# Optimization experiments

Hardware: AMD Instinct MI355X
Metric: run time of the kernel (lower is better)

The kernel has to match this reference:

```python
import jax, jax.numpy as jnp
import numpy as np

VOCAB = 100000
EMB = 256
HID = 512
H = HID // 2            # per-direction hidden size
T_LEN = 2048
N_TAGS = 7
START, END = 5, 6
NEG = -10000.0


def setup_inputs() -> dict:
    key = jax.random.key(0)
    ks = jax.random.split(key, 16)
    n = lambda k, sh: jax.random.normal(k, sh, dtype=jnp.float32)
    bound = 1.0 / np.sqrt(H)  # torch LSTM/Linear-style init scale
    u = lambda k, sh: jax.random.uniform(k, sh, dtype=jnp.float32, minval=-bound, maxval=bound)
    transitions = n(ks[12], (N_TAGS, N_TAGS))
    transitions = transitions.at[:, START].set(NEG).at[END, :].set(NEG)
    return {
        "words": jax.random.randint(ks[0], (T_LEN,), 0, VOCAB),
        "embed": n(ks[1], (VOCAB + 1, EMB)),
        "W_ih_f": u(ks[2], (4 * H, EMB)),
        "W_hh_f": u(ks[3], (4 * H, H)),
        "b_ih_f": u(ks[4], (4 * H,)),
        "b_hh_f": u(ks[5], (4 * H,)),
        "W_ih_b": u(ks[6], (4 * H, EMB)),
        "W_hh_b": u(ks[7], (4 * H, H)),
        "b_ih_b": u(ks[8], (4 * H,)),
        "b_hh_b": u(ks[9], (4 * H,)),
        "W_out": u(ks[10], (N_TAGS, HID)),
        "b_out": u(ks[11], (N_TAGS,)),
        "transitions": transitions,
        "h0": n(ks[13], (2, H)),
        "c0": n(ks[14], (2, H)),
    }


def _lstm_dir(xs, h0, c0, Wih, Whh, bih, bhh):
    # xs: [T, EMB]; torch gate order i, f, g, o
    def step(carry, x):
        h, c = carry
        g = x @ Wih.T + bih + h @ Whh.T + bhh  # [4H]
        i, f, gg, o = jnp.split(g, 4)
        i, f, o = jax.nn.sigmoid(i), jax.nn.sigmoid(f), jax.nn.sigmoid(o)
        c = f * c + i * jnp.tanh(gg)
        h = o * jnp.tanh(c)
        return (h, c), h
    _, hs = jax.lax.scan(step, (h0, c0), xs)
    return hs  # [T, H]


def _features(words, embed, W_ih_f, W_hh_f, b_ih_f, b_hh_f,
              W_ih_b, W_hh_b, b_ih_b, b_hh_b, W_out, b_out, h0, c0):
    xs = embed[words]                                   # [T, EMB]
    hs_f = _lstm_dir(xs, h0[0], c0[0], W_ih_f, W_hh_f, b_ih_f, b_hh_f)
    hs_b = _lstm_dir(xs[::-1], h0[1], c0[1], W_ih_b, W_hh_b, b_ih_b, b_hh_b)[::-1]
    lstm_out = jnp.concatenate([hs_f, hs_b], axis=1)    # [T, HID]
    return lstm_out @ W_out.T + b_out                   # [T, N_TAGS]


def _viterbi(feats, transitions):
    init = jnp.full((N_TAGS,), NEG, dtype=feats.dtype).at[START].set(0.0)

    def vit_step(fv, feat):
        # torch code: next_tag_var[j] = forward_var + transitions[j]
        M = fv[None, :] + transitions          # [j, i] = fv[i] + T[j, i]
        bp = jnp.argmax(M, axis=1)             # [N_TAGS] best prev tag
        fv_new = jnp.max(M, axis=1) + feat
        return fv_new, bp

    fv, bptrs = jax.lax.scan(vit_step, init, feats)     # bptrs: [T, N_TAGS]
    terminal = fv + transitions[END]
    final_tag = jnp.argmax(terminal)
    path_score = terminal[final_tag]

    def back_step(tag, bp):
        return bp[tag], tag
    _start, path = jax.lax.scan(back_step, final_tag, bptrs, reverse=True)
    return path_score, path  # path: [T] tag ids (B/I/E/S/N = 0..4)


def reference(words, embed, W_ih_f, W_hh_f, b_ih_f, b_hh_f,
              W_ih_b, W_hh_b, b_ih_b, b_hh_b, W_out, b_out,
              transitions, h0, c0):
    feats = _features(words, embed, W_ih_f, W_hh_f, b_ih_f, b_hh_f,
                      W_ih_b, W_hh_b, b_ih_b, b_hh_b, W_out, b_out, h0, c0)
    return _viterbi(feats, transitions)
```

## Files before the change

### kernel.cpp

```cpp
#include <hip/hip_runtime.h>

typedef unsigned int u32;

#define T_LEN 2048
#define NEG (-10000.0f)
#define WSCALE 2032.0f
#define HSCALE 127.0f
#define SCALE_INV (1.0f / (2032.0f * 127.0f))

__device__ __forceinline__ int sdot4(u32 a, u32 b, int c) {
#if __has_builtin(__builtin_amdgcn_sdot4)
  return __builtin_amdgcn_sdot4((int)a, (int)b, c, false);
#else
  int r = c;
  r += (int)(signed char)(a)       * (int)(signed char)(b);
  r += (int)(signed char)(a >> 8)  * (int)(signed char)(b >> 8);
  r += (int)(signed char)(a >> 16) * (int)(signed char)(b >> 16);
  r += (int)(signed char)(a >> 24) * (int)(signed char)(b >> 24);
  return r;
#endif
}

__device__ __forceinline__ u32 rdlane_u32(u32 v, int lane) {
#if __has_builtin(__builtin_amdgcn_readlane)
  return (u32)__builtin_amdgcn_readlane((int)v, lane);
#else
  return (u32)__shfl((int)v, lane);
#endif
}

__device__ __forceinline__ float rdlane_f32(float v, int lane) {
  return __builtin_bit_cast(float, rdlane_u32(__builtin_bit_cast(u32, v), lane));
}

__device__ __forceinline__ void block_sync_lds() {
  asm volatile("s_waitcnt lgkmcnt(0)" ::: "memory");
  __builtin_amdgcn_s_barrier();
}

__global__ void pack_whh_i8(const float* __restrict__ Wf,
                            const float* __restrict__ Wb,
                            u32* __restrict__ WP) {
  int idx = blockIdx.x * 256 + threadIdx.x;
  int d   = idx >> 16;
  int G   = (idx >> 14) & 3;
  int q4  = (idx >> 10) & 15;
  int c   = (idx >> 2) & 255;
  int j   = idx & 3;
  const float* W = d ? Wb : Wf;
  float4 v = *(const float4*)&W[(G * 256 + c) * 256 + q4 * 16 + j * 4];
  int b0 = (int)rintf(fminf(fmaxf(v.x * WSCALE, -127.f), 127.f));
  int b1 = (int)rintf(fminf(fmaxf(v.y * WSCALE, -127.f), 127.f));
  int b2 = (int)rintf(fminf(fmaxf(v.z * WSCALE, -127.f), 127.f));
  int b3 = (int)rintf(fminf(fmaxf(v.w * WSCALE, -127.f), 127.f));
  WP[(((d * 4 + G) * 16 + q4) * 256 + c) * 4 + j] =
      (u32)(b0 & 255) | ((u32)(b1 & 255) << 8) |
      ((u32)(b2 & 255) << 16) | ((u32)(b3 & 255) << 24);
}

__global__ void gather_kernel(const int* __restrict__ words,
                              const float* __restrict__ embed,
                              float* __restrict__ xs) {
  int t = blockIdx.x;
  int k = threadIdx.x;
  xs[t * 256 + k] = embed[(size_t)words[t] * 256 + k];
}

__global__ __launch_bounds__(256) void gemm_xw(
    const float* __restrict__ xs,
    const float* __restrict__ Wf, const float* __restrict__ Wb,
    const float* __restrict__ bihf, const float* __restrict__ bhhf,
    const float* __restrict__ bihb, const float* __restrict__ bhhb,
    float* __restrict__ XW) {
  __shared__ float lx[32 * 256];
  __shared__ float lw[32 * 132];
  const int tid = threadIdx.x;
  const int t0 = blockIdx.x * 32;
  const int g0 = blockIdx.y * 128;
  const int d  = blockIdx.z;
  const float* W = d ? Wb : Wf;

  #pragma unroll 4
  for (int r = 0; r < 32; ++r) lx[r * 256 + tid] = xs[(t0 + r) * 256 + tid];

  const int tg = tid & 31, tt = tid >> 5;
  float acc[4][4] = {};

  for (int kc = 0; kc < 8; ++kc) {
    __syncthreads();
    #pragma unroll
    for (int r2 = 0; r2 < 16; ++r2) {
      int gg = r2 * 8 + (tid >> 5);
      int k  = tid & 31;
      lw[k * 132 + gg] = W[(g0 + gg) * 256 + kc * 32 + k];
    }
    __syncthreads();
    #pragma unroll
    for (int k = 0; k < 32; ++k) {
      float4 wv = *(const float4*)&lw[k * 132 + tg * 4];
      #pragma unroll
      for (int a = 0; a < 4; ++a) {
        float xa = lx[(tt * 4 + a) * 256 + kc * 32 + k];
        acc[a][0] = fmaf(xa, wv.x, acc[a][0]);
        acc[a][1] = fmaf(xa, wv.y, acc[a][1]);
        acc[a][2] = fmaf(xa, wv.z, acc[a][2]);
        acc[a][3] = fmaf(xa, wv.w, acc[a][3]);
      }
    }
  }
  const float* bih = d ? bihb : bihf;
  const float* bhh = d ? bhhb : bhhf;
  int gcol = g0 + tg * 4;
  float4 bb;
  bb.x = bih[gcol + 0] + bhh[gcol + 0];
  bb.y = bih[gcol + 1] + bhh[gcol + 1];
  bb.z = bih[gcol + 2] + bhh[gcol + 2];
  bb.w = bih[gcol + 3] + bhh[gcol + 3];
  #pragma unroll
  for (int a = 0; a < 4; ++a) {
    float4 o;
    o.x = acc[a][0] + bb.x;
    o.y = acc[a][1] + bb.y;
    o.z = acc[a][2] + bb.z;
    o.w = acc[a][3] + bb.w;
    *(float4*)&XW[((size_t)d * T_LEN + t0 + tt * 4 + a) * 1024 + gcol] = o;
  }
}

__global__ void __launch_bounds__(256)
__attribute__((amdgpu_waves_per_eu(1, 1)))
lstm_seq(
    const float* __restrict__ XW, float* __restrict__ HS,
    const u32* __restrict__ wpack,
    const float* __restrict__ h0, const float* __restrict__ c0) {
  __shared__ u32 H8[2][64];
  const int tid = threadIdx.x;
  const int d = blockIdx.x;
  const int lane = tid & 63;

  u32 wIv[64], wFv[64], wGv[64], wOv[64];
  {
    const uint4* wr = (const uint4*)wpack;
    #pragma unroll
    for (int q4 = 0; q4 < 16; ++q4) {
      uint4 t;
      t = wr[((d * 4 + 0) * 16 + q4) * 256 + tid];
      wIv[q4 * 4 + 0] = t.x; wIv[q4 * 4 + 1] = t.y;
      wIv[q4 * 4 + 2] = t.z; wIv[q4 * 4 + 3] = t.w;
      t = wr[((d * 4 + 1) * 16 + q4) * 256 + tid];
      wFv[q4 * 4 + 0] = t.x; wFv[q4 * 4 + 1] = t.y;
      wFv[q4 * 4 + 2] = t.z; wFv[q4 * 4 + 3] = t.w;
      t = wr[((d * 4 + 2) * 16 + q4) * 256 + tid];
      wGv[q4 * 4 + 0] = t.x; wGv[q4 * 4 + 1] = t.y;
      wGv[q4 * 4 + 2] = t.z; wGv[q4 * 4 + 3] = t.w;
      t = wr[((d * 4 + 3) * 16 + q4) * 256 + tid];
      wOv[q4 * 4 + 0] = t.x; wOv[q4 * 4 + 1] = t.y;
      wOv[q4 * 4 + 2] = t.z; wOv[q4 * 4 + 3] = t.w;
    }
  }

  float c = c0[d * 256 + tid];
  float h = h0[d * 256 + tid];
  {
    int hi = (int)rintf(fminf(fmaxf(h, -1.0f), 1.0f) * HSCALE);
    ((unsigned char*)&H8[0][0])[tid] = (unsigned char)(hi & 255);
  }
  block_sync_lds();
  u32 hA = H8[0][lane];

  const int delta = d ? -1024 : 1024;
  const float* xwp = XW + ((size_t)d * T_LEN + (d ? (T_LEN - 1) : 0)) * 1024 + tid;
  float xi = xwp[0], xf = xwp[256], xg = xwp[512], xo = xwp[768];

  for (int s = 0; s < T_LEN; ++s) {
    float ni = 0.f, nf = 0.f, ng = 0.f, no = 0.f;
    if (s < T_LEN - 1) {
      xwp += delta;
      ni = xwp[0]; nf = xwp[256]; ng = xwp[512]; no = xwp[768];
    }

    int aI = 0, aF = 0, aG = 0, aO = 0;
    #pragma unroll
    for (int q = 0; q < 64; ++q) {
      u32 sv = rdlane_u32(hA, q);
      aI = sdot4(wIv[q], sv, aI);
      aF = sdot4(wFv[q], sv, aF);
      aG = sdot4(wGv[q], sv, aG);
      aO = sdot4(wOv[q], sv, aO);
    }

    float gi = fmaf((float)aI, SCALE_INV, xi);
    float gf = fmaf((float)aF, SCALE_INV, xf);
    float gc = fmaf((float)aG, SCALE_INV, xg);
    float go = fmaf((float)aO, SCALE_INV, xo);
    gi = 1.0f / (1.0f + __expf(-gi));
    gf = 1.0f / (1.0f + __expf(-gf));
    go = 1.0f / (1.0f + __expf(-go));
    gc = 1.0f - 2.0f / (__expf(2.0f * gc) + 1.0f);
    c = gf * c + gi * gc;
    float th = 1.0f - 2.0f / (__expf(2.0f * c) + 1.0f);
    h = go * th;

    const int t = d ? (T_LEN - 1 - s) : s;
    HS[((size_t)d * T_LEN + t) * 256 + tid] = h;

    int hi = (int)rintf(h * HSCALE);
    const int wbuf = (s + 1) & 1;
    ((unsigned char*)&H8[wbuf][0])[tid] = (unsigned char)(hi & 255);
    block_sync_lds();
    hA = H8[wbuf][lane];
    xi = ni; xf = nf; xg = ng; xo = no;
  }
}

__global__ void feats_kernel(const float* __restrict__ hs,
                             const float* __restrict__ wout,
                             const float* __restrict__ bout,
                             float* __restrict__ feats) {
  __shared__ float lf[16 * 257];
  __shared__ float lb[16 * 257];
  const int tid = threadIdx.x;
  const int t0 = blockIdx.x * 16;
  for (int i = tid; i < 16 * 256; i += 128) {
    int r = i >> 8, k = i & 255;
    lf[r * 257 + k] = hs[(size_t)(t0 + r) * 256 + k];
    lb[r * 257 + k] = hs[(size_t)T_LEN * 256 + (size_t)(t0 + r) * 256 + k];
  }
  __syncthreads();
  const int tl = tid >> 3, n = tid & 7;
  if (n < 7) {
    float acc = bout[n];
    #pragma unroll 8
    for (int k = 0; k < 256; ++k) acc = fmaf(lf[tl * 257 + k], wout[n * 512 + k], acc);
    #pragma unroll 8
    for (int k = 0; k < 256; ++k) acc = fmaf(lb[tl * 257 + k], wout[n * 512 + 256 + k], acc);
    feats[(t0 + tl) * 7 + n] = acc;
  }
}

__global__ __launch_bounds__(256) void viterbi_kernel(
    const float* __restrict__ feats,
    const float* __restrict__ trans,
    float* __restrict__ out) {
  extern __shared__ char vsm[];
  float*         fe = (float*)vsm;
  unsigned char* bp = (unsigned char*)(vsm + 57344);
  unsigned char* G  = (unsigned char*)(vsm + 73728);
  unsigned char* bt = (unsigned char*)(vsm + 73984);
  const int tid = threadIdx.x;

  for (int i = tid; i < T_LEN * 7; i += 256) fe[i] = feats[i];
  __syncthreads();

  if (tid < 64) {
    const int j  = tid;
    const int jc = (j < 7) ? j : 0;
    float Trow[7];
    #pragma unroll
    for (int i = 0; i < 7; ++i) Trow[i] = trans[jc * 7 + i];
    float fv = (j == 5) ? 0.0f : NEG;
    for (int t = 0; t < T_LEN; ++t) {
      float f0 = rdlane_f32(fv, 0), f1 = rdlane_f32(fv, 1), f2 = rdlane_f32(fv, 2),
            f3 = rdlane_f32(fv, 3), f4 = rdlane_f32(fv, 4), f5 = rdlane_f32(fv, 5),
            f6 = rdlane_f32(fv, 6);
      float v0 = f0 + Trow[0], v1 = f1 + Trow[1], v2 = f2 + Trow[2],
            v3 = f3 + Trow[3], v4 = f4 + Trow[4], v5 = f5 + Trow[5],
            v6 = f6 + Trow[6];
      bool c01 = v0 >= v1;  float m01 = c01 ? v0 : v1;  int i01 = c01 ? 0 : 1;
      bool c23 = v2 >= v3;  float m23 = c23 ? v2 : v3;  int i23 = c23 ? 2 : 3;
      bool c45 = v4 >= v5;  float m45 = c45 ? v4 : v5;  int i45 = c45 ? 4 : 5;
      bool cA  = m01 >= m23; float mA = cA ? m01 : m23; int iA = cA ? i01 : i23;
      bool cB  = m45 >= v6;  float mB = cB ? m45 : v6;  int iB = cB ? i45 : 6;
      bool cF  = mA >= mB;   float best = cF ? mA : mB; int bi = cF ? iA : iB;
      if (j < 7) bp[t * 8 + j] = (unsigned char)bi;
      fv = best + fe[t * 7 + jc];
    }
    float term = fv + trans[42 + jc];
    float best = rdlane_f32(term, 0); int btag = 0;
    #pragma unroll
    for (int i = 1; i < 7; ++i) {
      float ti = rdlane_f32(term, i);
      if (ti > best) { best = ti; btag = i; }
    }
    if (j == 0) {
      out[0] = best;
      bt[31] = (unsigned char)btag;
    }
  }
  __syncthreads();

  {
    const int s = tid >> 3, j = tid & 7;
    if (s < 32 && j < 7) {
      int g = j;
      for (int t = s * 64 + 63; t >= s * 64; --t) g = bp[t * 8 + g];
      G[s * 8 + j] = (unsigned char)g;
    }
  }
  __syncthreads();

  if (tid == 0) {
    int x = bt[31];
    for (int s = 31; s >= 1; --s) { x = G[s * 8 + x]; bt[s - 1] = (unsigned char)x; }
  }
  __syncthreads();

  if (tid < 32) {
    const int s = tid;
    int tag = bt[s];
    for (int t = s * 64 + 63; t >= s * 64; --t) {
      out[1 + t] = (float)tag;
      tag = bp[t * 8 + tag];
    }
  }
}

extern "C" void kernel_launch(void* const* d_in, const int* in_sizes, int n_in,
                              void* d_out, int out_size, void* d_ws, size_t ws_size,
                              hipStream_t stream) {
  const int*   words = (const int*)d_in[0];
  const float* embed = (const float*)d_in[1];
  const float* Wih_f = (const float*)d_in[2];
  const float* Whh_f = (const float*)d_in[3];
  const float* bih_f = (const float*)d_in[4];
  const float* bhh_f = (const float*)d_in[5];
  const float* Wih_b = (const float*)d_in[6];
  const float* Whh_b = (const float*)d_in[7];
  const float* bih_b = (const float*)d_in[8];
  const float* bhh_b = (const float*)d_in[9];
  const float* Wout  = (const float*)d_in[10];
  const float* bout  = (const float*)d_in[11];
  const float* trans = (const float*)d_in[12];
  const float* h0    = (const float*)d_in[13];
  const float* c0    = (const float*)d_in[14];

  float* ws = (float*)d_ws;
  float* XW = ws;
  float* HS = ws + 4194304;
  float* XS = ws + 5242880;
  float* FE = ws + 5767168;
  u32*   WP = (u32*)(ws + 5781504);

  pack_whh_i8<<<512, 256, 0, stream>>>(Whh_f, Whh_b, WP);
  gather_kernel<<<T_LEN, 256, 0, stream>>>(words, embed, XS);
  dim3 ggrid(T_LEN / 32, 1024 / 128, 2);
  gemm_xw<<<ggrid, 256, 0, stream>>>(XS, Wih_f, Wih_b, bih_f, bhh_f, bih_b, bhh_b, XW);
  lstm_seq<<<2, 256, 0, stream>>>(XW, HS, WP, h0, c0);
  feats_kernel<<<128, 128, 0, stream>>>(HS, Wout, bout, FE);
  viterbi_kernel<<<1, 256, 74048, stream>>>(FE, trans, (float*)d_out);
}
```

Measured before the change: 2.549 ms.

## Interleave gate pre-activations for float4 loads and pin int8 weights in VGPRs

The input-projection kernel now writes XW with the four gates of each hidden unit interleaved, so the recurrent kernel fetches one float4 per step instead of four strided scalar loads. Empty asm constraints pin the I/F/G weight arrays in VGPRs every iteration so the compiler cannot spill or rematerialize them. The dot-product loop is reordered to issue four readlanes before their sdot4 uses. The interleaved scalar stores in the projection kernel are less coalesced, and the O-gate weights are not pinned.

```diff
diff --git a/kernel.cpp b/kernel.cpp
--- a/kernel.cpp
+++ b/kernel.cpp
@@ -37,6 +37,13 @@
   asm volatile("s_waitcnt lgkmcnt(0)" ::: "memory");
   __builtin_amdgcn_s_barrier();
 }
+
+#define PIN8(a,b,c_,d_,e,f,g_,h_)                                     \
+  asm volatile("" : "+v"(a), "+v"(b), "+v"(c_), "+v"(d_),             \
+                    "+v"(e), "+v"(f), "+v"(g_), "+v"(h_))
+#define PINROW(W, base) \
+  PIN8(W[base+0], W[base+1], W[base+2], W[base+3],                    \
+       W[base+4], W[base+5], W[base+6], W[base+7])
 
 __global__ void pack_whh_i8(const float* __restrict__ Wf,
                             const float* __restrict__ Wb,
@@ -111,19 +118,17 @@
   const float* bih = d ? bihb : bihf;
   const float* bhh = d ? bhhb : bhhf;
   int gcol = g0 + tg * 4;
-  float4 bb;
-  bb.x = bih[gcol + 0] + bhh[gcol + 0];
-  bb.y = bih[gcol + 1] + bhh[gcol + 1];
-  bb.z = bih[gcol + 2] + bhh[gcol + 2];
-  bb.w = bih[gcol + 3] + bhh[gcol + 3];
+  float bb[4];
+  #pragma unroll
+  for (int j = 0; j < 4; ++j) bb[j] = bih[gcol + j] + bhh[gcol + j];
   #pragma unroll
   for (int a = 0; a < 4; ++a) {
-    float4 o;
-    o.x = acc[a][0] + bb.x;
-    o.y = acc[a][1] + bb.y;
-    o.z = acc[a][2] + bb.z;
-    o.w = acc[a][3] + bb.w;
-    *(float4*)&XW[((size_t)d * T_LEN + t0 + tt * 4 + a) * 1024 + gcol] = o;
+    size_t trow = (size_t)d * T_LEN + t0 + tt * 4 + a;
+    #pragma unroll
+    for (int j = 0; j < 4; ++j) {
+      int g = gcol + j;
+      XW[trow * 1024 + (g & 255) * 4 + (g >> 8)] = acc[a][j] + bb[j];
+    }
   }
 }
 
@@ -138,24 +143,20 @@
   const int d = blockIdx.x;
   const int lane = tid & 63;
 
-  u32 wIv[64], wFv[64], wGv[64], wOv[64];
+  u32 wI[64], wF[64], wG[64], wO[64];
   {
     const uint4* wr = (const uint4*)wpack;
     #pragma unroll
     for (int q4 = 0; q4 < 16; ++q4) {
       uint4 t;
       t = wr[((d * 4 + 0) * 16 + q4) * 256 + tid];
-      wIv[q4 * 4 + 0] = t.x; wIv[q4 * 4 + 1] = t.y;
-      wIv[q4 * 4 + 2] = t.z; wIv[q4 * 4 + 3] = t.w;
+      wI[q4*4+0] = t.x; wI[q4*4+1] = t.y; wI[q4*4+2] = t.z; wI[q4*4+3] = t.w;
       t = wr[((d * 4 + 1) * 16 + q4) * 256 + tid];
-      wFv[q4 * 4 + 0] = t.x; wFv[q4 * 4 + 1] = t.y;
-      wFv[q4 * 4 + 2] = t.z; wFv[q4 * 4 + 3] = t.w;
+      wF[q4*4+0] = t.x; wF[q4*4+1] = t.y; wF[q4*4+2] = t.z; wF[q4*4+3] = t.w;
       t = wr[((d * 4 + 2) * 16 + q4) * 256 + tid];
-      wGv[q4 * 4 + 0] = t.x; wGv[q4 * 4 + 1] = t.y;
-      wGv[q4 * 4 + 2] = t.z; wGv[q4 * 4 + 3] = t.w;
+      wG[q4*4+0] = t.x; wG[q4*4+1] = t.y; wG[q4*4+2] = t.z; wG[q4*4+3] = t.w;
       t = wr[((d * 4 + 3) * 16 + q4) * 256 + tid];
-      wOv[q4 * 4 + 0] = t.x; wOv[q4 * 4 + 1] = t.y;
-      wOv[q4 * 4 + 2] = t.z; wOv[q4 * 4 + 3] = t.w;
+      wO[q4*4+0] = t.x; wO[q4*4+1] = t.y; wO[q4*4+2] = t.z; wO[q4*4+3] = t.w;
     }
   }
 
@@ -169,30 +170,39 @@
   u32 hA = H8[0][lane];
 
   const int delta = d ? -1024 : 1024;
-  const float* xwp = XW + ((size_t)d * T_LEN + (d ? (T_LEN - 1) : 0)) * 1024 + tid;
-  float xi = xwp[0], xf = xwp[256], xg = xwp[512], xo = xwp[768];
+  const float* xwp = XW + ((size_t)d * T_LEN + (d ? (T_LEN - 1) : 0)) * 1024 + tid * 4;
+  float4 xc = *(const float4*)xwp;
 
   for (int s = 0; s < T_LEN; ++s) {
-    float ni = 0.f, nf = 0.f, ng = 0.f, no = 0.f;
-    if (s < T_LEN - 1) {
-      xwp += delta;
-      ni = xwp[0]; nf = xwp[256]; ng = xwp[512]; no = xwp[768];
-    }
+    float4 xn = make_float4(0.f, 0.f, 0.f, 0.f);
+    if (s < T_LEN - 1) { xwp += delta; xn = *(const float4*)xwp; }
+
+    PINROW(wI, 0);  PINROW(wI, 8);  PINROW(wI, 16); PINROW(wI, 24);
+    PINROW(wI, 32); PINROW(wI, 40); PINROW(wI, 48); PINROW(wI, 56);
+    PINROW(wF, 0);  PINROW(wF, 8);  PINROW(wF, 16); PINROW(wF, 24);
+    PINROW(wF, 32); PINROW(wF, 40); PINROW(wF, 48); PINROW(wF, 56);
+    PINROW(wG, 0);  PINROW(wG, 8);  PINROW(wG, 16); PINROW(wG, 24);
+    PINROW(wG, 32); PINROW(wG, 40); PINROW(wG, 48); PINROW(wG, 56);
 
     int aI = 0, aF = 0, aG = 0, aO = 0;
     #pragma unroll
-    for (int q = 0; q < 64; ++q) {
-      u32 sv = rdlane_u32(hA, q);
-      aI = sdot4(wIv[q], sv, aI);
-      aF = sdot4(wFv[q], sv, aF);
-      aG = sdot4(wGv[q], sv, aG);
-      aO = sdot4(wOv[q], sv, aO);
-    }
-
-    float gi = fmaf((float)aI, SCALE_INV, xi);
-    float gf = fmaf((float)aF, SCALE_INV, xf);
-    float gc = fmaf((float)aG, SCALE_INV, xg);
-    float go = fmaf((float)aO, SCALE_INV, xo);
+    for (int q = 0; q < 16; ++q) {
+      u32 s0 = rdlane_u32(hA, 4*q+0), s1 = rdlane_u32(hA, 4*q+1),
+          s2 = rdlane_u32(hA, 4*q+2), s3 = rdlane_u32(hA, 4*q+3);
+      aI = sdot4(wI[4*q+0], s0, aI); aF = sdot4(wF[4*q+0], s0, aF);
+      aG = sdot4(wG[4*q+0], s0, aG); aO = sdot4(wO[4*q+0], s0, aO);
+      aI = sdot4(wI[4*q+1], s1, aI); aF = sdot4(wF[4*q+1], s1, aF);
+      aG = sdot4(wG[4*q+1], s1, aG); aO = sdot4(wO[4*q+1], s1, aO);
+      aI = sdot4(wI[4*q+2], s2, aI); aF = sdot4(wF[4*q+2], s2, aF);
+      aG = sdot4(wG[4*q+2], s2, aG); aO = sdot4(wO[4*q+2], s2, aO);
+      aI = sdot4(wI[4*q+3], s3, aI); aF = sdot4(wF[4*q+3], s3, aF);
+      aG = sdot4(wG[4*q+3], s3, aG); aO = sdot4(wO[4*q+3], s3, aO);
+    }
+
+    float gi = fmaf((float)aI, SCALE_INV, xc.x);
+    float gf = fmaf((float)aF, SCALE_INV, xc.y);
+    float gc = fmaf((float)aG, SCALE_INV, xc.z);
+    float go = fmaf((float)aO, SCALE_INV, xc.w);
     gi = 1.0f / (1.0f + __expf(-gi));
     gf = 1.0f / (1.0f + __expf(-gf));
     go = 1.0f / (1.0f + __expf(-go));
@@ -209,7 +219,7 @@
     ((unsigned char*)&H8[wbuf][0])[tid] = (unsigned char)(hi & 255);
     block_sync_lds();
     hA = H8[wbuf][lane];
-    xi = ni; xf = nf; xg = ng; xo = no;
+    xc = xn;
   }
 }
 
```

Result: slower. 2.627 ms (+3.1%).
